# Kernel tuning notes

Hardware: AMD Instinct MI355X
Metric: run time of the kernel (lower is better)

Reference implementation:

```python
import jax, jax.numpy as jnp
import numpy as np

B, D, H, W = 8, 128, 152, 272
N_DET = 128
NHEAD = 8
DFF = 512


def _vis_pos_table(d):
    # PositionEmbeddingSine over the fixed 11-entry visibility grid [0,0.1,...,1.0]
    x_embed = jnp.arange(11, dtype=jnp.float32) * 0.1
    dim_t = jnp.arange(d, dtype=jnp.float32)
    dim_t = 10000.0 ** (2.0 * jnp.floor(dim_t / 2.0) / d)
    pos = x_embed[:, None] / dim_t  # [11, d]
    return jnp.stack([jnp.sin(pos[:, 0::2]), jnp.cos(pos[:, 1::2])], axis=2).reshape(11, d)


def _layer_norm(x, g, b, eps=1e-5):
    m = jnp.mean(x, axis=-1, keepdims=True)
    v = jnp.var(x, axis=-1, keepdims=True)
    return (x - m) / jnp.sqrt(v + eps) * g + b


def _adaptive_pool3(x, dets):
    # Faithful AdaptiveAvgPool2d(3) over per-detection crops, vectorized via integral image.
    # x: [B,D,H,W]; dets: [B,N,4] int boxes [x0,y0,x1,y1] with x1>x0, y1>y0.
    P = jnp.cumsum(jnp.cumsum(x, axis=2), axis=3)
    P = jnp.pad(P, ((0, 0), (0, 0), (1, 0), (1, 0)))  # [B,D,H+1,W+1]
    Pt = P.transpose(0, 2, 3, 1)  # [B,H+1,W+1,D]
    sx, sy, ex, ey = dets[..., 0], dets[..., 1], dets[..., 2], dets[..., 3]
    i = jnp.arange(3)

    def edges(s, e):
        # torch adaptive pool bins: start = floor(i*L/3), end = ceil((i+1)*L/3)
        L = (e - s)[..., None]
        st = s[..., None] + (i * L) // 3
        en = s[..., None] + -((-(i + 1) * L) // 3)
        return st, en

    ys, ye = edges(sy, ey)  # [B,N,3]
    xs, xe = edges(sx, ex)
    bidx = jnp.arange(x.shape[0])[:, None, None, None]
    Y0 = ys[:, :, :, None]; Y1 = ye[:, :, :, None]
    X0 = xs[:, :, None, :]; X1 = xe[:, :, None, :]
    g = lambda yy, xx: Pt[bidx, yy, xx]  # [B,N,3,3,D]
    s_ = g(Y1, X1) - g(Y0, X1) - g(Y1, X0) + g(Y0, X0)
    area = ((Y1 - Y0) * (X1 - X0)).astype(x.dtype)  # [B,N,3,3]
    return s_ / area[..., None]  # [B,N,3,3,D] (row-major y,x like .view(128,-1))


def setup_inputs() -> dict:
    key = jax.random.key(0)
    ks = jax.random.split(key, 12)
    x = jax.random.normal(ks[0], (B, D, H, W), jnp.float32)
    vis = jax.random.uniform(ks[1], (B, 1, H, W), jnp.float32)
    # boxes with guaranteed positive extents inside the clamp range (x<=271, y<=151)
    x0 = jax.random.randint(ks[2], (B, N_DET), 0, 230)
    y0 = jax.random.randint(ks[3], (B, N_DET), 0, 110)
    bw = jax.random.randint(ks[4], (B, N_DET), 3, 41)
    bh = jax.random.randint(ks[5], (B, N_DET), 3, 41)
    dets = jnp.stack([x0, y0, x0 + bw, y0 + bh], axis=-1).astype(jnp.int32)
    inds = jax.vmap(lambda k: jax.random.permutation(k, H * W)[:N_DET])(
        jax.random.split(ks[6], B)).astype(jnp.int32)
    s = 1.0 / np.sqrt(D).astype(np.float32)
    Wqkv = jax.random.normal(ks[7], (3 * D, D), jnp.float32) * s
    bqkv = jnp.zeros((3 * D,), jnp.float32)
    Wo = jax.random.normal(ks[8], (D, D), jnp.float32) * s
    bo = jnp.zeros((D,), jnp.float32)
    W1 = jax.random.normal(ks[9], (DFF, D), jnp.float32) * s
    b1 = jnp.zeros((DFF,), jnp.float32)
    W2 = jax.random.normal(ks[10], (D, DFF), jnp.float32) * np.float32(1.0 / np.sqrt(DFF))
    b2 = jnp.zeros((D,), jnp.float32)
    g2 = jnp.ones((D,), jnp.float32); be2 = jnp.zeros((D,), jnp.float32)
    g3 = jnp.ones((D,), jnp.float32); be3 = jnp.zeros((D,), jnp.float32)
    return dict(x=x, vis=vis, dets=dets, inds=inds, Wqkv=Wqkv, bqkv=bqkv, Wo=Wo, bo=bo,
                W1=W1, b1=b1, W2=W2, b2=b2, g2=g2, be2=be2, g3=g3, be3=be3)


def reference(x, vis, dets, inds, Wqkv, bqkv, Wo, bo, W1, b1, W2, b2, g2, be2, g3, be3):
    b, d, h, w = x.shape
    n = inds.shape[1]
    hd = d // NHEAD
    vis_pos = _vis_pos_table(d)  # [11, d]
    # --- query patches: gather point features at detection centers ---
    x_flat = x.transpose(0, 2, 3, 1).reshape(b, h * w, d)
    bidx = jnp.arange(b)[:, None]
    q = x_flat[bidx, inds]  # [b,n,d]
    vis_flat = vis.transpose(0, 2, 3, 1).reshape(b, h * w)
    vidx = (jax.lax.stop_gradient(vis_flat[bidx, inds]) * 10.0).astype(jnp.int32)  # [b,n] in [0,10]
    q = q + vis_pos[vidx]
    # --- key patches: 3x3 adaptive avg pool of each detection crop -> 9 tokens ---
    k = _adaptive_pool3(x, dets).reshape(b * n, 9, d)  # [bn,9,d]
    qf = q.reshape(b * n, 1, d)
    # --- nn.MultiheadAttention cross-attn: batch=b*n detections, L=1 query, S=9 keys ---
    Wq, Wk, Wv = Wqkv[:d], Wqkv[d:2 * d], Wqkv[2 * d:]
    bq, bk, bv = bqkv[:d], bqkv[d:2 * d], bqkv[2 * d:]
    qp = (qf @ Wq.T + bq).reshape(b * n, 1, NHEAD, hd)
    kp = (k @ Wk.T + bk).reshape(b * n, 9, NHEAD, hd)
    vp = (k @ Wv.T + bv).reshape(b * n, 9, NHEAD, hd)
    att = jnp.einsum('blhe,bshe->bhls', qp, kp) / jnp.sqrt(jnp.asarray(hd, x.dtype))
    att = jax.nn.softmax(att, axis=-1)
    ao = jnp.einsum('bhls,bshe->blhe', att, vp).reshape(b * n, 1, d)
    ao = ao @ Wo.T + bo
    # --- post-norm decoder layer (dropout=identity in eval) ---
    t = _layer_norm(qf + ao, g2, be2)
    t2 = jax.nn.relu(t @ W1.T + b1) @ W2.T + b2
    out = _layer_norm(t + t2, g3, be3).reshape(b, n, d)
    # --- scatter refined embeddings back into the feature map ---
    x_flat = x_flat.at[bidx, inds].set(out)
    return x_flat.reshape(b, h, w, d).transpose(0, 3, 1, 2)
```

## Files before the change

### kernel.cpp

```cpp
#include <hip/hip_runtime.h>
#include <math.h>

#define BB 8
#define CH 128
#define HH 152
#define WWID 272
#define HWSZ (HH*WWID)
#define NDET 128
#define NHEAD 8
#define HDIM 16
#define DFF 512
#define NDB (BB*NDET)
#define KSTRIDE 1152
#define CHUNK 16
#define RHALF 76
#define SROW 276
#define NTAIL 512
#define NCOPY 2048

typedef float f4v __attribute__((ext_vector_type(4)));

__device__ __forceinline__ float dot4(float4 w, float4 u, float s) {
    s = fmaf(w.x, u.x, s);
    s = fmaf(w.y, u.y, s);
    s = fmaf(w.z, u.z, s);
    s = fmaf(w.w, u.w, s);
    return s;
}

template<int CTRL, int RMASK>
__device__ __forceinline__ float dpp_add_step(float x) {
    int y = __builtin_amdgcn_update_dpp(0, __builtin_bit_cast(int, x),
                                        CTRL, RMASK, 0xf, false);
    return x + __builtin_bit_cast(float, y);
}
__device__ __forceinline__ float wave_incl_scan(float x) {
    x = dpp_add_step<0x111, 0xf>(x);
    x = dpp_add_step<0x112, 0xf>(x);
    x = dpp_add_step<0x114, 0xf>(x);
    x = dpp_add_step<0x118, 0xf>(x);
    x = dpp_add_step<0x142, 0xa>(x);
    x = dpp_add_step<0x143, 0xc>(x);
    return x;
}

__global__ __launch_bounds__(256) void pool_only(
    const float* __restrict__ x, const int* __restrict__ dets,
    float* __restrict__ kpart)
{
    const int bid   = blockIdx.x;
    const int t     = threadIdx.x;
    const int plane = bid >> 1, rhalf = bid & 1;
    const int b     = plane >> 7, ch = plane & 127;
    const int lane  = t & 63,  w  = t >> 6;
    const int rbeg  = rhalf * RHALF;

    __shared__ float S[CHUNK * SROW];

    const float* xp = x + ((size_t)b * CH + ch) * HWSZ;

    const int d = t & 127, half = t >> 7;
    const int4 dv = *((const int4*)(dets + (size_t)(b * NDET + d) * 4));
    const int sx = dv.x, sy = dv.y, ex = dv.z, ey = dv.w;
    const int Lx = ex - sx, Ly = ey - sy;
    const int xs1 = sx + Lx / 3,        xs2 = sx + 2 * Lx / 3;
    const int xe0 = sx + (Lx + 2) / 3,  xe1 = sx + (2 * Lx + 2) / 3;
    const int ys1 = sy + Ly / 3,        ys2 = sy + 2 * Ly / 3;
    const int ye0 = sy + (Ly + 2) / 3,  ye1 = sy + (2 * Ly + 2) / 3;

    float acc[9] = {0.f,0.f,0.f,0.f,0.f,0.f,0.f,0.f,0.f};

    #pragma unroll 1
    for (int cbeg = rbeg; cbeg < rbeg + RHALF; cbeg += CHUNK) {
        const int csize = (rbeg + RHALF - cbeg < CHUNK) ? (rbeg + RHALF - cbeg) : CHUNK;

        {
            int rl = w;
            f4v vm = (f4v)(0.f), ve = (f4v)(0.f);
            bool have = (rl < csize);
            if (have) {
                const f4v* rowp = (const f4v*)(xp + (size_t)(cbeg + rl) * WWID);
                vm = rowp[lane];
                if (lane < 4) ve = rowp[64 + lane];
            }
            while (have) {
                const int rc = rl;
                f4v v = vm, e = ve;
                rl += 4;
                have = (rl < csize);
                if (have) {
                    const f4v* rowp = (const f4v*)(xp + (size_t)(cbeg + rl) * WWID);
                    vm = rowp[lane];
                    if (lane < 4) ve = rowp[64 + lane];
                }
                float T = v[0] + v[1] + v[2] + v[3];
                float s = wave_incl_scan(T);
                float off0 = s - T;
                float* Sr = S + rc * SROW;
                f4v sm;
                sm[0] = off0;
                sm[1] = off0 + v[0];
                sm[2] = off0 + v[0] + v[1];
                sm[3] = off0 + v[0] + v[1] + v[2];
                *(f4v*)&Sr[4 * lane] = sm;
                float Te = (lane < 4) ? (e[0]+e[1]+e[2]+e[3]) : 0.f;
                float Tei = Te;
                Tei = dpp_add_step<0x111, 0xf>(Tei);
                Tei = dpp_add_step<0x112, 0xf>(Tei);
                float R    = __shfl(s, 63);
                float Esum = __shfl(Tei, 3);
                if (lane < 4) {
                    float offE = R + (Tei - Te);
                    f4v se;
                    se[0] = offE;
                    se[1] = offE + e[0];
                    se[2] = offE + e[0] + e[1];
                    se[3] = offE + e[0] + e[1] + e[2];
                    *(f4v*)&Sr[256 + 4 * lane] = se;
                }
                if (lane == 0) Sr[272] = R + Esum;
            }
        }
        __syncthreads();

        {
            int lo = (sy > cbeg) ? sy : cbeg;
            int hi = (ey < cbeg + csize) ? ey : (cbeg + csize);
            if (lo < hi) {
                int mid = (lo + hi + 1) >> 1;
                int y0 = half ? mid : lo;
                int y1 = half ? hi  : mid;
                for (int y = y0; y < y1; ++y) {
                    const float* Sr = S + (y - cbeg) * SROW;
                    float c0 = Sr[xe0] - Sr[sx];
                    float c1 = Sr[xe1] - Sr[xs1];
                    float c2 = Sr[ex]  - Sr[xs2];
                    float m0 = (y < ye0) ? 1.f : 0.f;
                    float m1 = (y >= ys1 && y < ye1) ? 1.f : 0.f;
                    float m2 = (y >= ys2) ? 1.f : 0.f;
                    acc[0] = fmaf(m0, c0, acc[0]); acc[1] = fmaf(m0, c1, acc[1]); acc[2] = fmaf(m0, c2, acc[2]);
                    acc[3] = fmaf(m1, c0, acc[3]); acc[4] = fmaf(m1, c1, acc[4]); acc[5] = fmaf(m1, c2, acc[5]);
                    acc[6] = fmaf(m2, c0, acc[6]); acc[7] = fmaf(m2, c1, acc[7]); acc[8] = fmaf(m2, c2, acc[8]);
                }
            }
        }
        __syncthreads();
    }

    if (half) {
        #pragma unroll
        for (int j = 0; j < 9; ++j) S[d * 9 + j] = acc[j];
    }
    __syncthreads();
    if (!half) {
        float* kd = kpart + ((size_t)rhalf * NDB + (size_t)(b * NDET + d)) * KSTRIDE + ch;
        #pragma unroll
        for (int j = 0; j < 9; ++j)
            kd[j * CH] = acc[j] + S[d * 9 + j];
    }
}

__global__ __launch_bounds__(256) void tail_copy(
    const float* __restrict__ x, const float* __restrict__ vis,
    const int* __restrict__ dets, const int* __restrict__ inds,
    const float* __restrict__ kpA, const float* __restrict__ kpB,
    const float* __restrict__ Wqkv, const float* __restrict__ bqkv,
    const float* __restrict__ Wo,   const float* __restrict__ bo,
    const float* __restrict__ W1,   const float* __restrict__ b1,
    const float* __restrict__ W2,   const float* __restrict__ b2,
    const float* __restrict__ g2,   const float* __restrict__ be2,
    const float* __restrict__ g3,   const float* __restrict__ be3,
    float* __restrict__ rowsb, float* __restrict__ out)
{
    const int bid = blockIdx.x;
    const int t   = threadIdx.x;

    if (bid >= NTAIL) {
        const size_t n4 = (size_t)BB * CH * HWSZ / 4;
        const f4v* s4 = (const f4v*)x;
        f4v* o4 = (f4v*)out;
        size_t i = (size_t)(bid - NTAIL) * 256 + t;
        const size_t stride = (size_t)NCOPY * 256;
        for (; i < n4; i += stride) {
            f4v v = s4[i];
            __builtin_nontemporal_store(v, &o4[i]);
        }
        return;
    }

    const int d0  = bid * 2;
    const int b   = d0 >> 7;
    const int o   = t & 127, dl = t >> 7;

    __shared__ float kbuf[2 * 9 * CH];
    __shared__ float kp[2 * 9 * CH];
    __shared__ float vp[2 * 9 * CH];
    __shared__ float invA[2][9];
    __shared__ float qv[2][CH];
    __shared__ float qp[2][CH];
    __shared__ float attl[2][NHEAD][9];
    __shared__ float aov[2][CH];
    __shared__ float Tv[2][CH];
    __shared__ float h1[2][DFF];
    __shared__ float part2[2][2][CH];
    __shared__ float wst[4][2];

    if (t < 18) {
        int dd = t / 9, slot = t - dd * 9;
        const int4 dv = *((const int4*)(dets + (size_t)(b * NDET + ((d0 + dd) & 127)) * 4));
        int sx = dv.x, sy = dv.y, ex = dv.z, ey = dv.w;
        int Lx = ex - sx, Ly = ey - sy;
        int xs1 = sx + Lx / 3,       xs2 = sx + 2 * Lx / 3;
        int xe0 = sx + (Lx + 2) / 3, xe1 = sx + (2 * Lx + 2) / 3;
        int ys1 = sy + Ly / 3,       ys2 = sy + 2 * Ly / 3;
        int ye0 = sy + (Ly + 2) / 3, ye1 = sy + (2 * Ly + 2) / 3;
        int xi = slot % 3, yi = slot / 3;
        int wdt = (xi == 0) ? (xe0 - sx) : (xi == 1) ? (xe1 - xs1) : (ex - xs2);
        int hgt = (yi == 0) ? (ye0 - sy) : (yi == 1) ? (ye1 - ys1) : (ey - ys2);
        invA[dd][slot] = 1.0f / (float)(hgt * wdt);
    }
    {
        int p = inds[b * NDET + ((d0 + dl) & 127)];
        float qval = x[((size_t)b * CH + o) * HWSZ + p];
        float vv   = vis[(size_t)b * HWSZ + p];
        int vidx   = (int)(vv * 10.0f);
        float fr   = powf(10000.0f, -(float)(o & 126) * (1.0f / 128.0f));
        float ang  = 0.1f * (float)vidx * fr;
        qv[dl][o]  = qval + ((o & 1) ? cosf(ang) : sinf(ang));
    }
    __syncthreads();

    for (int i = t; i < 2 * KSTRIDE; i += 256) {
        int dd = (i >= KSTRIDE);
        int r  = i - dd * KSTRIDE;
        int slot = r >> 7;
        float vA = kpA[(size_t)(d0 + dd) * KSTRIDE + r];
        float vB = kpB[(size_t)(d0 + dd) * KSTRIDE + r];
        kbuf[dd * KSTRIDE + r] = (vA + vB) * invA[dd][slot];
    }
    __syncthreads();

    {
        const float4* wr = (const float4*)(Wqkv + (size_t)o * CH);
        const float4* qq = (const float4*)&qv[dl][0];
        float s = 0.f;
        #pragma unroll 8
        for (int i = 0; i < 32; ++i) s = dot4(wr[i], qq[i], s);
        qp[dl][o] = s + bqkv[o];
    }
    {
        const int which = t >> 7;
        const float4* wr = (const float4*)(Wqkv + (size_t)(CH + which * CH + o) * CH);
        float acc[18];
        #pragma unroll
        for (int r = 0; r < 18; ++r) acc[r] = 0.f;
        for (int i = 0; i < 32; ++i) {
            float4 w = wr[i];
            #pragma unroll
            for (int r = 0; r < 18; ++r) {
                float4 a = ((const float4*)kbuf)[r * 32 + i];
                acc[r] = dot4(w, a, acc[r]);
            }
        }
        const float bias = bqkv[CH + which * CH + o];
        float* dst = which ? vp : kp;
        #pragma unroll
        for (int r = 0; r < 18; ++r) dst[r * CH + o] = acc[r] + bias;
    }
    __syncthreads();

    if (o < 72) {
        int h = o / 9, s = o - h * 9;
        const float* qh = &qp[dl][h * HDIM];
        const float* kh = &kp[dl * KSTRIDE + s * CH + h * HDIM];
        float a = 0.f;
        #pragma unroll
        for (int e = 0; e < HDIM; ++e) a = fmaf(qh[e], kh[e], a);
        attl[dl][h][s] = a * 0.25f;
    }
    __syncthreads();
    if (o < 8) {
        float m = attl[dl][o][0];
        #pragma unroll
        for (int s = 1; s < 9; ++s) m = fmaxf(m, attl[dl][o][s]);
        float e[9]; float sum = 0.f;
        #pragma unroll
        for (int s = 0; s < 9; ++s) { e[s] = expf(attl[dl][o][s] - m); sum += e[s]; }
        float inv = 1.0f / sum;
        #pragma unroll
        for (int s = 0; s < 9; ++s) attl[dl][o][s] = e[s] * inv;
    }
    __syncthreads();
    {
        int h = o >> 4;
        float a = 0.f;
        #pragma unroll
        for (int s = 0; s < 9; ++s) a = fmaf(attl[dl][h][s], vp[dl * KSTRIDE + s * CH + o], a);
        aov[dl][o] = a;
    }
    __syncthreads();

    float v1;
    {
        const float4* wr = (const float4*)(Wo + (size_t)o * CH);
        const float4* u4 = (const float4*)&aov[dl][0];
        float s = 0.f;
        #pragma unroll 8
        for (int i = 0; i < 32; ++i) s = dot4(wr[i], u4[i], s);
        v1 = qv[dl][o] + s + bo[o];
    }
    {
        float s1 = v1, s2 = v1 * v1;
        #pragma unroll
        for (int off = 32; off >= 1; off >>= 1) {
            s1 += __shfl_xor(s1, off);
            s2 += __shfl_xor(s2, off);
        }
        if ((t & 63) == 0) { wst[t >> 6][0] = s1; wst[t >> 6][1] = s2; }
    }
    __syncthreads();
    {
        float sum = wst[2 * dl][0] + wst[2 * dl + 1][0];
        float sq  = wst[2 * dl][1] + wst[2 * dl + 1][1];
        float m   = sum * (1.0f / 128.0f);
        float var = sq  * (1.0f / 128.0f) - m * m;
        Tv[dl][o] = (v1 - m) * rsqrtf(var + 1e-5f) * g2[o] + be2[o];
    }
    __syncthreads();

    #pragma unroll
    for (int rep = 0; rep < 2; ++rep) {
        int oo = t + rep * 256;
        const float4* wr = (const float4*)(W1 + (size_t)oo * CH);
        float a0 = 0.f, a1 = 0.f;
        for (int i = 0; i < 32; ++i) {
            float4 w = wr[i];
            a0 = dot4(w, ((const float4*)&Tv[0][0])[i], a0);
            a1 = dot4(w, ((const float4*)&Tv[1][0])[i], a1);
        }
        float bb = b1[oo];
        h1[0][oo] = fmaxf(a0 + bb, 0.f);
        h1[1][oo] = fmaxf(a1 + bb, 0.f);
    }
    __syncthreads();

    {
        const int hf = t >> 7;
        const float4* wr = (const float4*)(W2 + (size_t)o * DFF + hf * (DFF / 2));
        float a0 = 0.f, a1 = 0.f;
        #pragma unroll 4
        for (int i = 0; i < 64; ++i) {
            float4 w = wr[i];
            a0 = dot4(w, ((const float4*)&h1[0][hf * 256])[i], a0);
            a1 = dot4(w, ((const float4*)&h1[1][hf * 256])[i], a1);
        }
        part2[hf][0][o] = a0;
        part2[hf][1][o] = a1;
    }
    __syncthreads();
    float v2 = part2[0][dl][o] + part2[1][dl][o] + b2[o] + Tv[dl][o];
    {
        float s1 = v2, s2 = v2 * v2;
        #pragma unroll
        for (int off = 32; off >= 1; off >>= 1) {
            s1 += __shfl_xor(s1, off);
            s2 += __shfl_xor(s2, off);
        }
        if ((t & 63) == 0) { wst[t >> 6][0] = s1; wst[t >> 6][1] = s2; }
    }
    __syncthreads();
    {
        float sum = wst[2 * dl][0] + wst[2 * dl + 1][0];
        float sq  = wst[2 * dl][1] + wst[2 * dl + 1][1];
        float m   = sum * (1.0f / 128.0f);
        float var = sq  * (1.0f / 128.0f) - m * m;
        float ov  = (v2 - m) * rsqrtf(var + 1e-5f) * g3[o] + be3[o];
        rowsb[(size_t)(d0 + dl) * CH + o] = ov;
    }
}

__global__ __launch_bounds__(256) void scatter_rows(const float* __restrict__ rows,
                                                    const int* __restrict__ inds,
                                                    float* __restrict__ out) {
    int i = blockIdx.x * 256 + threadIdx.x;
    int dd = i & (CH - 1);
    int bn = i >> 7;
    int b  = bn >> 7;
    int p  = inds[bn];
    out[((size_t)b * CH + dd) * HWSZ + p] = rows[i];
}

__global__ __launch_bounds__(256) void copy_x(const f4v* __restrict__ src,
                                              f4v* __restrict__ dst, size_t n4) {
    size_t i = (size_t)blockIdx.x * 256 + threadIdx.x;
    const size_t stride = (size_t)gridDim.x * 256;
    for (; i < n4; i += stride) {
        f4v v = src[i];
        __builtin_nontemporal_store(v, &dst[i]);
    }
}

__device__ __forceinline__ float block_layernorm(float v, int t,
        const float* __restrict__ gamma, const float* __restrict__ beta,
        float* redA, float* redB) {
    float s1 = v, s2 = v * v;
    #pragma unroll
    for (int off = 32; off >= 1; off >>= 1) {
        s1 += __shfl_xor(s1, off);
        s2 += __shfl_xor(s2, off);
    }
    if ((t & 63) == 0) { redA[t >> 6] = s1; redB[t >> 6] = s2; }
    __syncthreads();
    float sum = redA[0] + redA[1] + redA[2] + redA[3];
    float sq  = redB[0] + redB[1] + redB[2] + redB[3];
    __syncthreads();
    float m   = sum * (1.0f / 128.0f);
    float var = sq  * (1.0f / 128.0f) - m * m;
    float r = 0.f;
    if (t < CH) r = (v - m) * rsqrtf(var + 1e-5f) * gamma[t] + beta[t];
    return r;
}

__global__ __launch_bounds__(256) void er_fused_fb(
    const float* __restrict__ x, const float* __restrict__ vis,
    const int* __restrict__ dets, const int* __restrict__ inds,
    const float* __restrict__ Wqkv, const float* __restrict__ bqkv,
    const float* __restrict__ Wo,   const float* __restrict__ bo,
    const float* __restrict__ W1,   const float* __restrict__ b1,
    const float* __restrict__ W2,   const float* __restrict__ b2,
    const float* __restrict__ g2,   const float* __restrict__ be2,
    const float* __restrict__ g3,   const float* __restrict__ be3,
    float* __restrict__ out)
{
    const int bid = blockIdx.x;
    const int t   = threadIdx.x;

    __shared__ float kbuf[9][CH];
    __shared__ float qv[CH];
    __shared__ float qp[CH];
    __shared__ float kp[9][CH];
    __shared__ float vp[9][CH];
    __shared__ float att[NHEAD][9];
    __shared__ float aov[CH];
    __shared__ float tv[CH];
    __shared__ float h1[DFF];
    __shared__ float part[256];
    __shared__ float redA[4], redB[4];
    __shared__ float msk[48][4];

    const int b = bid >> 7;
    const int n = bid & (NDET - 1);

    const int4 dv = *((const int4*)(dets + (size_t)(b * NDET + n) * 4));
    const int sx = dv.x, sy = dv.y, ex = dv.z, ey = dv.w;
    const int Lx = ex - sx, Ly = ey - sy;
    const int xs1 = sx + Lx / 3,        xs2 = sx + 2 * Lx / 3;
    const int xe0 = sx + (Lx + 2) / 3,  xe1 = sx + (2 * Lx + 2) / 3;
    const int ys1 = sy + Ly / 3,        ys2 = sy + 2 * Ly / 3;
    const int ye0 = sy + (Ly + 2) / 3,  ye1 = sy + (2 * Ly + 2) / 3;

    const int p = inds[b * NDET + n];

    if (t < 48) {
        int y = sy + t;
        bool inb = (y < ey);
        msk[t][0] = (inb && y < ye0)              ? 1.f : 0.f;
        msk[t][1] = (inb && y >= ys1 && y < ye1)  ? 1.f : 0.f;
        msk[t][2] = (inb && y >= ys2)             ? 1.f : 0.f;
        msk[t][3] = 0.f;
    }
    if (t < CH) {
        float qval = x[((size_t)b * CH + t) * HWSZ + p];
        float vv   = vis[(size_t)b * HWSZ + p];
        int vidx   = (int)(vv * 10.0f);
        float fr   = powf(10000.0f, -(float)(t & 126) * (1.0f / 128.0f));
        float ang  = 0.1f * (float)vidx * fr;
        float pe   = (t & 1) ? cosf(ang) : sinf(ang);
        qv[t] = qval + pe;
    }
    __syncthreads();

    {
        const int g   = t >> 4;
        const int lx  = t & 15;
        const int sx4 = sx & ~3;
        const int xb  = sx4 + lx * 4;
        const int lxmax = ((ex - 1) - sx4) >> 2;
        const int xba = sx4 + ((lx < lxmax) ? lx : lxmax) * 4;

        float4 mx0, mx1, mx2;
        {
            float m0[4], m1[4], m2[4];
            #pragma unroll
            for (int e = 0; e < 4; ++e) {
                int xx = xb + e;
                m0[e] = (xx >= sx  && xx < xe0) ? 1.f : 0.f;
                m1[e] = (xx >= xs1 && xx < xe1) ? 1.f : 0.f;
                m2[e] = (xx >= xs2 && xx < ex ) ? 1.f : 0.f;
            }
            mx0 = make_float4(m0[0], m0[1], m0[2], m0[3]);
            mx1 = make_float4(m1[0], m1[1], m1[2], m1[3]);
            mx2 = make_float4(m2[0], m2[1], m2[2], m2[3]);
        }

        const int rows_n = ey - sy;
        const int nch    = (rows_n + 7) >> 3;

        for (int c = 0; c < 8; ++c) {
            const int dd = g + c * 16;
            const float* base = x + ((size_t)b * CH + dd) * HWSZ + xba;
            float4 ac0 = make_float4(0.f,0.f,0.f,0.f);
            float4 ac1 = make_float4(0.f,0.f,0.f,0.f);
            float4 ac2 = make_float4(0.f,0.f,0.f,0.f);
            for (int ck = 0; ck < nch; ++ck) {
                const int y0 = sy + (ck << 3);
                float4 v[8];
                #pragma unroll
                for (int k = 0; k < 8; ++k) {
                    int y = y0 + k;
                    y = (y < ey) ? y : (ey - 1);
                    v[k] = *(const float4*)(base + (size_t)y * WWID);
                }
                #pragma unroll
                for (int k = 0; k < 8; ++k) {
                    const float4 m = *(const float4*)&msk[(y0 - sy) + k][0];
                    ac0.x = fmaf(m.x, v[k].x, ac0.x); ac0.y = fmaf(m.x, v[k].y, ac0.y);
                    ac0.z = fmaf(m.x, v[k].z, ac0.z); ac0.w = fmaf(m.x, v[k].w, ac0.w);
                    ac1.x = fmaf(m.y, v[k].x, ac1.x); ac1.y = fmaf(m.y, v[k].y, ac1.y);
                    ac1.z = fmaf(m.y, v[k].z, ac1.z); ac1.w = fmaf(m.y, v[k].w, ac1.w);
                    ac2.x = fmaf(m.z, v[k].x, ac2.x); ac2.y = fmaf(m.z, v[k].y, ac2.y);
                    ac2.z = fmaf(m.z, v[k].z, ac2.z); ac2.w = fmaf(m.z, v[k].w, ac2.w);
                }
            }
            float a[9];
            a[0] = dot4(mx0, ac0, 0.f); a[1] = dot4(mx1, ac0, 0.f); a[2] = dot4(mx2, ac0, 0.f);
            a[3] = dot4(mx0, ac1, 0.f); a[4] = dot4(mx1, ac1, 0.f); a[5] = dot4(mx2, ac1, 0.f);
            a[6] = dot4(mx0, ac2, 0.f); a[7] = dot4(mx1, ac2, 0.f); a[8] = dot4(mx2, ac2, 0.f);
            #pragma unroll
            for (int jj = 0; jj < 9; ++jj) {
                a[jj] += __shfl_xor(a[jj], 8);
                a[jj] += __shfl_xor(a[jj], 4);
                a[jj] += __shfl_xor(a[jj], 2);
                a[jj] += __shfl_xor(a[jj], 1);
            }
            if (lx == 0) {
                int w0 = xe0 - sx, w1 = xe1 - xs1, w2 = ex - xs2;
                int h0 = ye0 - sy, h1r = ye1 - ys1, h2 = ey - ys2;
                kbuf[0][dd] = a[0] / (float)(h0 * w0);
                kbuf[1][dd] = a[1] / (float)(h0 * w1);
                kbuf[2][dd] = a[2] / (float)(h0 * w2);
                kbuf[3][dd] = a[3] / (float)(h1r * w0);
                kbuf[4][dd] = a[4] / (float)(h1r * w1);
                kbuf[5][dd] = a[5] / (float)(h1r * w2);
                kbuf[6][dd] = a[6] / (float)(h2 * w0);
                kbuf[7][dd] = a[7] / (float)(h2 * w1);
                kbuf[8][dd] = a[8] / (float)(h2 * w2);
            }
        }
    }
    __syncthreads();

    if (t < CH) {
        const float4* wr = (const float4*)(Wqkv + (size_t)t * CH);
        const float4* qq = (const float4*)qv;
        float s = 0.f;
        #pragma unroll 8
        for (int i = 0; i < CH / 4; ++i) s = dot4(wr[i], qq[i], s);
        qp[t] = s + bqkv[t];
    }
    {
        const int o = t & (CH - 1);
        const int which = t >> 7;
        const float4* wr = (const float4*)(Wqkv + (size_t)(CH + which * CH + o) * CH);
        float acc[9] = {0.f,0.f,0.f,0.f,0.f,0.f,0.f,0.f,0.f};
        #pragma unroll 4
        for (int i = 0; i < CH / 4; ++i) {
            float4 w = wr[i];
            #pragma unroll
            for (int s = 0; s < 9; ++s) {
                float4 kk = ((const float4*)(&kbuf[s][0]))[i];
                acc[s] = dot4(w, kk, acc[s]);
            }
        }
        float bias = bqkv[CH + which * CH + o];
        if (which == 0) {
            #pragma unroll
            for (int s = 0; s < 9; ++s) kp[s][o] = acc[s] + bias;
        } else {
            #pragma unroll
            for (int s = 0; s < 9; ++s) vp[s][o] = acc[s] + bias;
        }
    }
    __syncthreads();

    if (t < NHEAD * 9) {
        int h = t / 9, s = t - h * 9;
        const float* qh = qp + h * HDIM;
        const float* kh = &kp[s][h * HDIM];
        float a = 0.f;
        #pragma unroll
        for (int e = 0; e < HDIM; ++e) a = fmaf(qh[e], kh[e], a);
        att[h][s] = a * 0.25f;
    }
    __syncthreads();

    if (t < NHEAD) {
        float m = att[t][0];
        #pragma unroll
        for (int s = 1; s < 9; ++s) m = fmaxf(m, att[t][s]);
        float e[9]; float sum = 0.f;
        #pragma unroll
        for (int s = 0; s < 9; ++s) { e[s] = expf(att[t][s] - m); sum += e[s]; }
        float inv = 1.0f / sum;
        #pragma unroll
        for (int s = 0; s < 9; ++s) att[t][s] = e[s] * inv;
    }
    __syncthreads();

    if (t < CH) {
        int h = t >> 4;
        float a = 0.f;
        #pragma unroll
        for (int s = 0; s < 9; ++s) a = fmaf(att[h][s], vp[s][t], a);
        aov[t] = a;
    }
    __syncthreads();

    float v1 = 0.f;
    if (t < CH) {
        const float4* wr = (const float4*)(Wo + (size_t)t * CH);
        const float4* u4 = (const float4*)aov;
        float s = 0.f;
        #pragma unroll 8
        for (int i = 0; i < CH / 4; ++i) s = dot4(wr[i], u4[i], s);
        v1 = qv[t] + s + bo[t];
    }
    float t1 = block_layernorm(v1, t, g2, be2, redA, redB);
    if (t < CH) tv[t] = t1;
    __syncthreads();

    #pragma unroll
    for (int rep = 0; rep < 2; ++rep) {
        int o = t + rep * 256;
        const float4* wr = (const float4*)(W1 + (size_t)o * CH);
        const float4* u4 = (const float4*)tv;
        float s = 0.f;
        #pragma unroll 8
        for (int i = 0; i < CH / 4; ++i) s = dot4(wr[i], u4[i], s);
        h1[o] = fmaxf(s + b1[o], 0.f);
    }
    __syncthreads();

    {
        int o = t & (CH - 1), hf = t >> 7;
        const float4* wr = (const float4*)(W2 + (size_t)o * DFF + hf * (DFF / 2));
        const float4* u4 = (const float4*)(h1 + hf * (DFF / 2));
        float s = 0.f;
        #pragma unroll 8
        for (int i = 0; i < DFF / 8; ++i) s = dot4(wr[i], u4[i], s);
        part[t] = s;
    }
    __syncthreads();

    float v2 = 0.f;
    if (t < CH) {
        float t2 = part[t] + part[t + 128] + b2[t];
        v2 = tv[t] + t2;
    }
    float outv = block_layernorm(v2, t, g3, be3, redA, redB);
    if (t < CH) out[((size_t)b * CH + t) * HWSZ + p] = outv;
}

extern "C" void kernel_launch(void* const* d_in, const int* in_sizes, int n_in,
                              void* d_out, int out_size, void* d_ws, size_t ws_size,
                              hipStream_t stream) {
    const float* x    = (const float*)d_in[0];
    const float* vis  = (const float*)d_in[1];
    const int*   dets = (const int*)d_in[2];
    const int*   inds = (const int*)d_in[3];
    const float* Wqkv = (const float*)d_in[4];
    const float* bqkv = (const float*)d_in[5];
    const float* Wo   = (const float*)d_in[6];
    const float* bo   = (const float*)d_in[7];
    const float* W1   = (const float*)d_in[8];
    const float* b1   = (const float*)d_in[9];
    const float* W2   = (const float*)d_in[10];
    const float* b2   = (const float*)d_in[11];
    const float* g2   = (const float*)d_in[12];
    const float* be2  = (const float*)d_in[13];
    const float* g3   = (const float*)d_in[14];
    const float* be3  = (const float*)d_in[15];
    float* out = (float*)d_out;

    const size_t SZ_KP   = (size_t)NDB * KSTRIDE;
    const size_t SZ_ROWS = (size_t)NDB * CH;
    const size_t need = (2 * SZ_KP + SZ_ROWS) * sizeof(float);

    const size_t N4 = (size_t)BB * CH * HWSZ / 4;
    if (ws_size >= need) {
        float* kpA  = (float*)d_ws;
        float* kpB  = kpA + SZ_KP;
        float* rows = kpB + SZ_KP;

        pool_only<<<dim3(2048), dim3(256), 0, stream>>>(x, dets, kpA);
        tail_copy<<<dim3(NTAIL + NCOPY), dim3(256), 0, stream>>>(
            x, vis, dets, inds, kpA, kpB, Wqkv, bqkv, Wo, bo,
            W1, b1, W2, b2, g2, be2, g3, be3, rows, out);
        scatter_rows<<<dim3((NDB * CH) / 256), dim3(256), 0, stream>>>(
            rows, inds, out);
    } else {
        copy_x<<<dim3(2048), dim3(256), 0, stream>>>(
            (const f4v*)x, (f4v*)out, N4);
        er_fused_fb<<<dim3(NDB), dim3(256), 0, stream>>>(
            x, vis, dets, inds, Wqkv, bqkv, Wo, bo, W1, b1, W2, b2,
            g2, be2, g3, be3, out);
    }
}
```

Baseline: 152.0 us.

## Process one detection per block instead of two in fused attention tail

The fused attention/FFN tail kernel now gives each block a single detection instead of two, doubling the number of tail blocks (NTAIL 512 to 1024) and halving per-block shared memory and register accumulators. This is meant to raise parallelism and occupancy so the tail spreads across more CUs alongside the copy blocks. In exchange, each weight row loaded from global/L2 is reused for only one detection instead of two, doubling weight traffic, and half the threads sit idle in several 128-wide phases.

```diff
diff --git a/kernel.cpp b/kernel.cpp
--- a/kernel.cpp
+++ b/kernel.cpp
@@ -15,7 +15,7 @@
 #define CHUNK 16
 #define RHALF 76
 #define SROW 276
-#define NTAIL 512
+#define NTAIL 1024
 #define NCOPY 2048
 
 typedef float f4v __attribute__((ext_vector_type(4)));
@@ -188,76 +188,72 @@
         return;
     }
 
-    const int d0  = bid * 2;
-    const int b   = d0 >> 7;
-    const int o   = t & 127, dl = t >> 7;
-
-    __shared__ float kbuf[2 * 9 * CH];
-    __shared__ float kp[2 * 9 * CH];
-    __shared__ float vp[2 * 9 * CH];
-    __shared__ float invA[2][9];
-    __shared__ float qv[2][CH];
-    __shared__ float qp[2][CH];
-    __shared__ float attl[2][NHEAD][9];
-    __shared__ float aov[2][CH];
-    __shared__ float Tv[2][CH];
-    __shared__ float h1[2][DFF];
-    __shared__ float part2[2][2][CH];
-    __shared__ float wst[4][2];
-
-    if (t < 18) {
-        int dd = t / 9, slot = t - dd * 9;
-        const int4 dv = *((const int4*)(dets + (size_t)(b * NDET + ((d0 + dd) & 127)) * 4));
+    const int det = bid;
+    const int b   = det >> 7;
+    const int o   = t & 127;
+
+    __shared__ float kbuf[KSTRIDE];
+    __shared__ float kp[KSTRIDE];
+    __shared__ float vp[KSTRIDE];
+    __shared__ float invA[9];
+    __shared__ float qv[CH];
+    __shared__ float qp[CH];
+    __shared__ float attl[NHEAD][9];
+    __shared__ float aov[CH];
+    __shared__ float Tv[CH];
+    __shared__ float h1[DFF];
+    __shared__ float part2[2][CH];
+    __shared__ float wst[2][2];
+
+    if (t < 9) {
+        const int4 dv = *((const int4*)(dets + (size_t)det * 4));
         int sx = dv.x, sy = dv.y, ex = dv.z, ey = dv.w;
         int Lx = ex - sx, Ly = ey - sy;
         int xs1 = sx + Lx / 3,       xs2 = sx + 2 * Lx / 3;
         int xe0 = sx + (Lx + 2) / 3, xe1 = sx + (2 * Lx + 2) / 3;
         int ys1 = sy + Ly / 3,       ys2 = sy + 2 * Ly / 3;
         int ye0 = sy + (Ly + 2) / 3, ye1 = sy + (2 * Ly + 2) / 3;
-        int xi = slot % 3, yi = slot / 3;
+        int xi = t % 3, yi = t / 3;
         int wdt = (xi == 0) ? (xe0 - sx) : (xi == 1) ? (xe1 - xs1) : (ex - xs2);
         int hgt = (yi == 0) ? (ye0 - sy) : (yi == 1) ? (ye1 - ys1) : (ey - ys2);
-        invA[dd][slot] = 1.0f / (float)(hgt * wdt);
-    }
-    {
-        int p = inds[b * NDET + ((d0 + dl) & 127)];
-        float qval = x[((size_t)b * CH + o) * HWSZ + p];
+        invA[t] = 1.0f / (float)(hgt * wdt);
+    }
+    if (t < CH) {
+        int p = inds[det];
+        float qval = x[((size_t)b * CH + t) * HWSZ + p];
         float vv   = vis[(size_t)b * HWSZ + p];
         int vidx   = (int)(vv * 10.0f);
-        float fr   = powf(10000.0f, -(float)(o & 126) * (1.0f / 128.0f));
+        float fr   = powf(10000.0f, -(float)(t & 126) * (1.0f / 128.0f));
         float ang  = 0.1f * (float)vidx * fr;
-        qv[dl][o]  = qval + ((o & 1) ? cosf(ang) : sinf(ang));
-    }
-    __syncthreads();
-
-    for (int i = t; i < 2 * KSTRIDE; i += 256) {
-        int dd = (i >= KSTRIDE);
-        int r  = i - dd * KSTRIDE;
-        int slot = r >> 7;
-        float vA = kpA[(size_t)(d0 + dd) * KSTRIDE + r];
-        float vB = kpB[(size_t)(d0 + dd) * KSTRIDE + r];
-        kbuf[dd * KSTRIDE + r] = (vA + vB) * invA[dd][slot];
-    }
-    __syncthreads();
-
-    {
+        qv[t] = qval + ((t & 1) ? cosf(ang) : sinf(ang));
+    }
+    __syncthreads();
+
+    for (int i = t; i < KSTRIDE; i += 256) {
+        float vA = kpA[(size_t)det * KSTRIDE + i];
+        float vB = kpB[(size_t)det * KSTRIDE + i];
+        kbuf[i] = (vA + vB) * invA[i >> 7];
+    }
+    __syncthreads();
+
+    if (t < CH) {
         const float4* wr = (const float4*)(Wqkv + (size_t)o * CH);
-        const float4* qq = (const float4*)&qv[dl][0];
+        const float4* qq = (const float4*)qv;
         float s = 0.f;
         #pragma unroll 8
         for (int i = 0; i < 32; ++i) s = dot4(wr[i], qq[i], s);
-        qp[dl][o] = s + bqkv[o];
+        qp[o] = s + bqkv[o];
     }
     {
         const int which = t >> 7;
         const float4* wr = (const float4*)(Wqkv + (size_t)(CH + which * CH + o) * CH);
-        float acc[18];
-        #pragma unroll
-        for (int r = 0; r < 18; ++r) acc[r] = 0.f;
+        float acc[9];
+        #pragma unroll
+        for (int r = 0; r < 9; ++r) acc[r] = 0.f;
         for (int i = 0; i < 32; ++i) {
             float4 w = wr[i];
             #pragma unroll
-            for (int r = 0; r < 18; ++r) {
+            for (int r = 0; r < 9; ++r) {
                 float4 a = ((const float4*)kbuf)[r * 32 + i];
                 acc[r] = dot4(w, a, acc[r]);
             }
@@ -265,49 +261,49 @@
         const float bias = bqkv[CH + which * CH + o];
         float* dst = which ? vp : kp;
         #pragma unroll
-        for (int r = 0; r < 18; ++r) dst[r * CH + o] = acc[r] + bias;
-    }
-    __syncthreads();
-
-    if (o < 72) {
-        int h = o / 9, s = o - h * 9;
-        const float* qh = &qp[dl][h * HDIM];
-        const float* kh = &kp[dl * KSTRIDE + s * CH + h * HDIM];
+        for (int r = 0; r < 9; ++r) dst[r * CH + o] = acc[r] + bias;
+    }
+    __syncthreads();
+
+    if (t < NHEAD * 9) {
+        int h = t / 9, s = t - h * 9;
+        const float* qh = qp + h * HDIM;
+        const float* kh = kp + s * CH + h * HDIM;
         float a = 0.f;
         #pragma unroll
         for (int e = 0; e < HDIM; ++e) a = fmaf(qh[e], kh[e], a);
-        attl[dl][h][s] = a * 0.25f;
-    }
-    __syncthreads();
-    if (o < 8) {
-        float m = attl[dl][o][0];
-        #pragma unroll
-        for (int s = 1; s < 9; ++s) m = fmaxf(m, attl[dl][o][s]);
+        attl[h][s] = a * 0.25f;
+    }
+    __syncthreads();
+    if (t < NHEAD) {
+        float m = attl[t][0];
+        #pragma unroll
+        for (int s = 1; s < 9; ++s) m = fmaxf(m, attl[t][s]);
         float e[9]; float sum = 0.f;
         #pragma unroll
-        for (int s = 0; s < 9; ++s) { e[s] = expf(attl[dl][o][s] - m); sum += e[s]; }
+        for (int s = 0; s < 9; ++s) { e[s] = expf(attl[t][s] - m); sum += e[s]; }
         float inv = 1.0f / sum;
         #pragma unroll
-        for (int s = 0; s < 9; ++s) attl[dl][o][s] = e[s] * inv;
-    }
-    __syncthreads();
-    {
-        int h = o >> 4;
+        for (int s = 0; s < 9; ++s) attl[t][s] = e[s] * inv;
+    }
+    __syncthreads();
+    if (t < CH) {
+        int h = t >> 4;
         float a = 0.f;
         #pragma unroll
-        for (int s = 0; s < 9; ++s) a = fmaf(attl[dl][h][s], vp[dl * KSTRIDE + s * CH + o], a);
-        aov[dl][o] = a;
-    }
-    __syncthreads();
-
-    float v1;
-    {
+        for (int s = 0; s < 9; ++s) a = fmaf(attl[h][s], vp[s * CH + t], a);
+        aov[t] = a;
+    }
+    __syncthreads();
+
+    float v1 = 0.f;
+    if (t < CH) {
         const float4* wr = (const float4*)(Wo + (size_t)o * CH);
-        const float4* u4 = (const float4*)&aov[dl][0];
+        const float4* u4 = (const float4*)aov;
         float s = 0.f;
         #pragma unroll 8
         for (int i = 0; i < 32; ++i) s = dot4(wr[i], u4[i], s);
-        v1 = qv[dl][o] + s + bo[o];
+        v1 = qv[o] + s + bo[o];
     }
     {
         float s1 = v1, s2 = v1 * v1;
@@ -316,15 +312,15 @@
             s1 += __shfl_xor(s1, off);
             s2 += __shfl_xor(s2, off);
         }
-        if ((t & 63) == 0) { wst[t >> 6][0] = s1; wst[t >> 6][1] = s2; }
-    }
-    __syncthreads();
-    {
-        float sum = wst[2 * dl][0] + wst[2 * dl + 1][0];
-        float sq  = wst[2 * dl][1] + wst[2 * dl + 1][1];
+        if (t < CH && (t & 63) == 0) { wst[t >> 6][0] = s1; wst[t >> 6][1] = s2; }
+    }
+    __syncthreads();
+    if (t < CH) {
+        float sum = wst[0][0] + wst[1][0];
+        float sq  = wst[0][1] + wst[1][1];
         float m   = sum * (1.0f / 128.0f);
         float var = sq  * (1.0f / 128.0f) - m * m;
-        Tv[dl][o] = (v1 - m) * rsqrtf(var + 1e-5f) * g2[o] + be2[o];
+        Tv[o] = (v1 - m) * rsqrtf(var + 1e-5f) * g2[o] + be2[o];
     }
     __syncthreads();
 
@@ -332,33 +328,25 @@
     for (int rep = 0; rep < 2; ++rep) {
         int oo = t + rep * 256;
         const float4* wr = (const float4*)(W1 + (size_t)oo * CH);
-        float a0 = 0.f, a1 = 0.f;
-        for (int i = 0; i < 32; ++i) {
-            float4 w = wr[i];
-            a0 = dot4(w, ((const float4*)&Tv[0][0])[i], a0);
-            a1 = dot4(w, ((const float4*)&Tv[1][0])[i], a1);
-        }
-        float bb = b1[oo];
-        h1[0][oo] = fmaxf(a0 + bb, 0.f);
-        h1[1][oo] = fmaxf(a1 + bb, 0.f);
+        const float4* u4 = (const float4*)Tv;
+        float s = 0.f;
+        for (int i = 0; i < 32; ++i) s = dot4(wr[i], u4[i], s);
+        h1[oo] = fmaxf(s + b1[oo], 0.f);
     }
     __syncthreads();
 
     {
         const int hf = t >> 7;
         const float4* wr = (const float4*)(W2 + (size_t)o * DFF + hf * (DFF / 2));
-        float a0 = 0.f, a1 = 0.f;
+        const float4* u4 = (const float4*)(h1 + hf * (DFF / 2));
+        float s = 0.f;
         #pragma unroll 4
-        for (int i = 0; i < 64; ++i) {
-            float4 w = wr[i];
-            a0 = dot4(w, ((const float4*)&h1[0][hf * 256])[i], a0);
-            a1 = dot4(w, ((const float4*)&h1[1][hf * 256])[i], a1);
-        }
-        part2[hf][0][o] = a0;
-        part2[hf][1][o] = a1;
-    }
-    __syncthreads();
-    float v2 = part2[0][dl][o] + part2[1][dl][o] + b2[o] + Tv[dl][o];
+        for (int i = 0; i < 64; ++i) s = dot4(wr[i], u4[i], s);
+        part2[hf][o] = s;
+    }
+    __syncthreads();
+    float v2 = 0.f;
+    if (t < CH) v2 = part2[0][o] + part2[1][o] + b2[o] + Tv[o];
     {
         float s1 = v2, s2 = v2 * v2;
         #pragma unroll
@@ -366,16 +354,16 @@
             s1 += __shfl_xor(s1, off);
             s2 += __shfl_xor(s2, off);
         }
-        if ((t & 63) == 0) { wst[t >> 6][0] = s1; wst[t >> 6][1] = s2; }
-    }
-    __syncthreads();
-    {
-        float sum = wst[2 * dl][0] + wst[2 * dl + 1][0];
-        float sq  = wst[2 * dl][1] + wst[2 * dl + 1][1];
+        if (t < CH && (t & 63) == 0) { wst[t >> 6][0] = s1; wst[t >> 6][1] = s2; }
+    }
+    __syncthreads();
+    if (t < CH) {
+        float sum = wst[0][0] + wst[1][0];
+        float sq  = wst[0][1] + wst[1][1];
         float m   = sum * (1.0f / 128.0f);
         float var = sq  * (1.0f / 128.0f) - m * m;
         float ov  = (v2 - m) * rsqrtf(var + 1e-5f) * g3[o] + be3[o];
-        rowsb[(size_t)(d0 + dl) * CH + o] = ov;
+        rowsb[(size_t)det * CH + o] = ov;
     }
 }
 
```

Result: slower. 189.7 us (+24.8%).
